# Kernel optimization log

Measured on AMD Instinct MI355X. Metric: run time of the kernel, lower is better.

Reference implementation:

```python
import jax, jax.numpy as jnp
import numpy as np

N_NODES = 50000
N_EDGES = 800000
IN_DIM = 16
HID = 128
OUT_DIM = 1
N_LAYERS = 2


def setup_inputs() -> dict:
    key = jax.random.key(0)
    ks = jax.random.split(key, 16)
    s = 0.05
    inp = {
        "edge_feats": jax.random.normal(ks[0], (N_EDGES, IN_DIM), jnp.float32),
        "node_feats": jax.random.normal(ks[1], (N_NODES, 4), jnp.float32),
        "src": jax.random.randint(ks[2], (N_EDGES,), 0, N_NODES, jnp.int32),
        "dst": jax.random.randint(ks[3], (N_EDGES,), 0, N_NODES, jnp.int32),
        # edge_embedding (dead in original forward, kept for faithfulness)
        "W_eemb": jax.random.normal(ks[4], (IN_DIM, HID), jnp.float32) * s,
        "b_eemb": jnp.zeros((HID,), jnp.float32),
        # node_embedding: Linear(4, hidden)
        "W_nemb": jax.random.normal(ks[5], (4, HID), jnp.float32) * s,
        "b_nemb": jnp.zeros((HID,), jnp.float32),
        # stacked GraphConv weights [n_layers, H, H]
        "gnn_W": jax.random.normal(ks[6], (N_LAYERS, HID, HID), jnp.float32) * s,
        "gnn_b": jnp.zeros((N_LAYERS, HID), jnp.float32),
        # output MLP
        "out_W1": jax.random.normal(ks[7], (HID, HID), jnp.float32) * s,
        "out_b1": jnp.zeros((HID,), jnp.float32),
        "out_W2": jax.random.normal(ks[8], (HID, OUT_DIM), jnp.float32) * s,
        "out_b2": jnp.zeros((OUT_DIM,), jnp.float32),
    }
    return inp


def reference(edge_feats, node_feats, src, dst, W_eemb, b_eemb, W_nemb, b_nemb,
              gnn_W, gnn_b, out_W1, out_b1, out_W2, out_b2):
    ones = jnp.ones((src.shape[0],), jnp.float32)
    deg_out = jnp.clip(jax.ops.segment_sum(ones, src, num_segments=N_NODES), 1.0)
    deg_in = jnp.clip(jax.ops.segment_sum(ones, dst, num_segments=N_NODES), 1.0)
    norm_out = deg_out ** -0.5  # [N]
    norm_in = deg_in ** -0.5    # [N]

    # edge_embedding output is dead code in the original forward (overwritten)
    _h_e = edge_feats @ W_eemb + b_eemb

    h = node_feats @ W_nemb + b_nemb  # [N, H]
    for l in range(N_LAYERS):
        # DGL GraphConv norm='both': D_out^{-1/2} gather -> scatter-sum -> D_in^{-1/2} -> W, b
        hs = h * norm_out[:, None]
        agg = jax.ops.segment_sum(hs[src], dst, num_segments=N_NODES)  # [N, H]
        h = agg * norm_in[:, None]
        h = h @ gnn_W[l] + gnn_b[l]
        h = jax.nn.relu(h)

    edge_h = h[src] + h[dst]  # apply_edges UDF, [E, H]
    x = jax.nn.relu(edge_h @ out_W1 + out_b1)
    return x @ out_W2 + out_b2  # [E, OUT_DIM]
```

## Files before the change

### kernel.cpp

```cpp
#include <hip/hip_runtime.h>

#define N_NODES 50000
#define N_EDGES 800000
#define HID 128
#define NB 256
#define NPB 196
#define TP 136

typedef __attribute__((ext_vector_type(8))) _Float16 f16x8;
typedef __attribute__((ext_vector_type(2))) _Float16 h2v;
typedef __attribute__((ext_vector_type(2))) __fp16 fp16v2;
typedef __attribute__((ext_vector_type(4))) float f32x4;
typedef __attribute__((ext_vector_type(2))) float f32x2;

__device__ __forceinline__ unsigned pkh(float a, float b) {
  union { fp16v2 h; unsigned u; } c;
  c.h = __builtin_amdgcn_cvt_pkrtz(a, b);
  return c.u;
}
__device__ __forceinline__ h2v u2h(unsigned u) {
  union { unsigned u; h2v h; } c;
  c.u = u;
  return c.h;
}
__device__ __forceinline__ f32x2 unpkh(unsigned u) {
  h2v h = u2h(u);
  f32x2 r;
  r[0] = (float)h[0];
  r[1] = (float)h[1];
  return r;
}
__device__ __forceinline__ short f2hs(float f) {
  union { _Float16 h; short s; } c;
  c.h = (_Float16)f;
  return c.s;
}
__device__ __forceinline__ unsigned hrelu_add(unsigned a, unsigned b) {
  h2v r = u2h(a) + u2h(b);
  h2v z = {(_Float16)0.f, (_Float16)0.f};
  r = __builtin_elementwise_max(r, z);
  union { h2v h; unsigned u; } c;
  c.h = r;
  return c.u;
}


__global__ __launch_bounds__(256) void p1_hist_kernel(
    const int* __restrict__ src, const int* __restrict__ dst,
    int* __restrict__ bcnt_d, int* __restrict__ bcnt_s) {
  __shared__ int hd[NB], hs[NB];
  int t = threadIdx.x;
  hd[t] = 0; hs[t] = 0;
  __syncthreads();
  for (int e = blockIdx.x * 256 + t; e < N_EDGES; e += gridDim.x * 256) {
    atomicAdd(&hd[dst[e] / NPB], 1);
    atomicAdd(&hs[src[e] / NPB], 1);
  }
  __syncthreads();
  if (hd[t]) atomicAdd(&bcnt_d[t], hd[t]);
  if (hs[t]) atomicAdd(&bcnt_s[t], hs[t]);
}

__global__ void p2_scan_prep_kernel(
    const int* __restrict__ bcnt_d, const int* __restrict__ bcnt_s,
    int* __restrict__ bofs_d, int* __restrict__ bofs_s,
    int* __restrict__ cur_d, int* __restrict__ cur_s,
    const float* __restrict__ Wa, const float* __restrict__ Wb,
    const float* __restrict__ Wc, const float* __restrict__ w2f,
    short* __restrict__ Wta, short* __restrict__ Wtb, short* __restrict__ Wtc,
    unsigned* __restrict__ w2h, short* __restrict__ h1bz) {
  int b = blockIdx.x;
  if (b > 0) {
    int t = (b - 1) * 256 + threadIdx.x;
    if (t < HID * HID) {
      int k = t >> 7, n = t & 127;
      Wta[n * HID + k] = f2hs(Wa[t]);
      Wtb[n * HID + k] = f2hs(Wb[t]);
      Wtc[n * HID + k] = f2hs(Wc[t]);
    }
    if (b == 1) {
      int t0 = threadIdx.x;
      if (t0 < 64) {
        w2h[t0] = pkh(w2f[2 * t0], w2f[2 * t0 + 1]);
      } else if (t0 < 128) {
        ((unsigned*)h1bz)[t0 - 64] = 0u;
      }
    }
    return;
  }
  __shared__ int s[NB];
  int t = threadIdx.x;
  int v = bcnt_d[t];
  s[t] = v;
  __syncthreads();
  for (int o = 1; o < NB; o <<= 1) {
    int x = (t >= o) ? s[t - o] : 0;
    __syncthreads();
    s[t] += x;
    __syncthreads();
  }
  int ofs = s[t] - v;
  bofs_d[t] = ofs; cur_d[t] = ofs;
  if (t == NB - 1) bofs_d[NB] = s[t];
  __syncthreads();
  v = bcnt_s[t];
  s[t] = v;
  __syncthreads();
  for (int o = 1; o < NB; o <<= 1) {
    int x = (t >= o) ? s[t - o] : 0;
    __syncthreads();
    s[t] += x;
    __syncthreads();
  }
  ofs = s[t] - v;
  bofs_s[t] = ofs; cur_s[t] = ofs;
  if (t == NB - 1) bofs_s[NB] = s[t];
}

__global__ __launch_bounds__(256) void p3_scatter_both_kernel(
    const int* __restrict__ src, const int* __restrict__ dst,
    int* __restrict__ cur_d, int* __restrict__ cur_s,
    int2* __restrict__ sdst, int* __restrict__ ssrc) {
  __shared__ int bcd[NB], bbd[NB], bcs[NB], bbs[NB];
  int t = threadIdx.x;
  int base = blockIdx.x * 2048;
  bcd[t] = 0; bcs[t] = 0;
  __syncthreads();
  int mybd[8], myrd[8], mys[8], myp[8], mybs[8], myrs[8];
#pragma unroll
  for (int u = 0; u < 8; ++u) {
    int e = base + u * 256 + t;
    mybd[u] = -1;
    if (e < N_EDGES) {
      int s = src[e], d = dst[e];
      int bd = d / NPB;
      mybd[u] = bd;
      myrd[u] = atomicAdd(&bcd[bd], 1);
      mys[u] = s;
      myp[u] = ((d - bd * NPB) << 20) | e;
      int bs = s / NPB;
      mybs[u] = bs;
      myrs[u] = atomicAdd(&bcs[bs], 1);
    }
  }
  __syncthreads();
  {
    int cd = bcd[t];
    if (cd) bbd[t] = atomicAdd(&cur_d[t], cd);
    int cs = bcs[t];
    if (cs) bbs[t] = atomicAdd(&cur_s[t], cs);
  }
  __syncthreads();
#pragma unroll
  for (int u = 0; u < 8; ++u) {
    if (mybd[u] >= 0) {
      sdst[bbd[mybd[u]] + myrd[u]] = make_int2(mys[u], myp[u]);
      ssrc[bbs[mybs[u]] + myrs[u]] = mys[u];
    }
  }
}

__global__ __launch_bounds__(256) void p45_kernel(
    const int2* __restrict__ sdst, const int* __restrict__ bofs_d,
    int* __restrict__ row_ofs, float* __restrict__ norm_in,
    int* __restrict__ csr_src, int* __restrict__ csr_eid, int* __restrict__ csr_dst,
    const int* __restrict__ ssrc, const int* __restrict__ bofs_s,
    float* __restrict__ norm_out) {
  __shared__ int hc[NB], sc[NB], cur[NB];
  int t = threadIdx.x;
  if (blockIdx.x >= NB) {
    int b = blockIdx.x - NB;
    int base = bofs_s[b], cnt = bofs_s[b + 1] - base;
    int lo = b * NPB;
    hc[t] = 0;
    __syncthreads();
    for (int i = t; i < cnt; i += 256) atomicAdd(&hc[ssrc[base + i] - lo], 1);
    __syncthreads();
    int node = lo + t;
    if (t < NPB && node < N_NODES) {
      int v = hc[t];
      norm_out[node] = rsqrtf((float)(v < 1 ? 1 : v));
    }
    return;
  }
  int b = blockIdx.x;
  int base = bofs_d[b], cnt = bofs_d[b + 1] - base;
  hc[t] = 0;
  __syncthreads();
  for (int i = t; i < cnt; i += 256) atomicAdd(&hc[sdst[base + i].y >> 20], 1);
  __syncthreads();
  int v = hc[t];
  sc[t] = v;
  __syncthreads();
  for (int o = 1; o < NB; o <<= 1) {
    int x = (t >= o) ? sc[t - o] : 0;
    __syncthreads();
    sc[t] += x;
    __syncthreads();
  }
  int ofs = sc[t] - v;
  int node = b * NPB + t;
  if (t < NPB && node < N_NODES) {
    row_ofs[node] = base + ofs;
    norm_in[node] = rsqrtf((float)(v < 1 ? 1 : v));
  }
  cur[t] = base + ofs;
  if (b == 0 && t == 0) row_ofs[N_NODES] = N_EDGES;
  __syncthreads();
  for (int i = t; i < cnt; i += 256) {
    int2 e = sdst[base + i];
    int loc = e.y >> 20;
    int pos = atomicAdd(&cur[loc], 1);
    csr_src[pos] = e.x;
    csr_eid[pos] = e.y & 0xFFFFF;
    csr_dst[pos] = b * NPB + loc;
  }
}


__global__ __launch_bounds__(256) void agg4_kernel(
    const float4* __restrict__ nf4, const float* __restrict__ no_,
    const int* __restrict__ csr_src, const int* __restrict__ row_ofs,
    float4* __restrict__ agg4, float* __restrict__ sno) {
  int wid = (blockIdx.x * blockDim.x + threadIdx.x) >> 6;
  int lane = threadIdx.x & 63;
  int g = lane >> 4, l = lane & 15;
  int v = wid * 4 + g;
  if (v >= N_NODES) return;
  int beg = row_ofs[v], end = row_ofs[v + 1];
  float ax = 0.f, ay = 0.f, az = 0.f, aw = 0.f, sn = 0.f;
  for (int i = beg + l; i < end; i += 16) {
    int s = csr_src[i];
    float w = no_[s];
    float4 n = nf4[s];
    ax += n.x * w; ay += n.y * w; az += n.z * w; aw += n.w * w;
    sn += w;
  }
#pragma unroll
  for (int o = 1; o < 16; o <<= 1) {
    ax += __shfl_xor(ax, o, 16);
    ay += __shfl_xor(ay, o, 16);
    az += __shfl_xor(az, o, 16);
    aw += __shfl_xor(aw, o, 16);
    sn += __shfl_xor(sn, o, 16);
  }
  if (l == 0) {
    agg4[v] = make_float4(ax, ay, az, aw);
    sno[v] = sn;
  }
}

__global__ __launch_bounds__(256) void gemm_l1_mfma(
    const float4* __restrict__ agg4, const float* __restrict__ sno,
    const float* __restrict__ ni_, const float* __restrict__ no_,
    const float* __restrict__ Wn, const float* __restrict__ bn,
    const short* __restrict__ Wt0, const float* __restrict__ b0,
    short* __restrict__ h1b, int nrows) {
  int t = threadIdx.x;
  int w = t >> 6, lane = t & 63;
  int m16 = lane & 15, quad = lane >> 4;
  int v0 = blockIdx.x * 64;
  int row = v0 + w * 16 + m16;
  bool rvalid = row < nrows;
  int rc = rvalid ? row : (nrows - 1);
  float4 a = agg4[rc];
  float sn = sno[rc], nin = ni_[rc];

  f16x8 xfr[4];
#pragma unroll
  for (int kc = 0; kc < 4; ++kc) {
    union { unsigned u[4]; f16x8 v; } cv;
#pragma unroll
    for (int jj = 0; jj < 4; ++jj) {
      int k0 = kc * 32 + quad * 8 + jj * 2;
      float x0 = (a.x * Wn[k0] + a.y * Wn[HID + k0] + a.z * Wn[2 * HID + k0] +
                  a.w * Wn[3 * HID + k0] + bn[k0] * sn) * nin;
      int k1 = k0 + 1;
      float x1 = (a.x * Wn[k1] + a.y * Wn[HID + k1] + a.z * Wn[2 * HID + k1] +
                  a.w * Wn[3 * HID + k1] + bn[k1] * sn) * nin;
      cv.u[jj] = pkh(x0, x1);
    }
    xfr[kc] = cv.v;
  }
  f32x4 acc[8];
#pragma unroll
  for (int nt = 0; nt < 8; ++nt) {
    acc[nt][0] = 0.f; acc[nt][1] = 0.f; acc[nt][2] = 0.f; acc[nt][3] = 0.f;
  }
#pragma unroll
  for (int nt = 0; nt < 8; ++nt) {
    const f16x8* Wr = (const f16x8*)(Wt0 + (size_t)(nt * 16 + m16) * HID);
#pragma unroll
    for (int kc = 0; kc < 4; ++kc)
      acc[nt] = __builtin_amdgcn_mfma_f32_16x16x32_f16(Wr[kc * 4 + quad], xfr[kc],
                                                       acc[nt], 0, 0, 0);
  }
  if (rvalid) {
    float nov = no_[row];
#pragma unroll
    for (int nt = 0; nt < 8; ++nt) {
      int nb = nt * 16 + quad * 4;
      float4 bv = *(const float4*)&b0[nb];
      float r0 = fmaxf(acc[nt][0] + bv.x, 0.f) * nov;
      float r1 = fmaxf(acc[nt][1] + bv.y, 0.f) * nov;
      float r2 = fmaxf(acc[nt][2] + bv.z, 0.f) * nov;
      float r3 = fmaxf(acc[nt][3] + bv.w, 0.f) * nov;
      uint2 pk;
      pk.x = pkh(r0, r1);
      pk.y = pkh(r2, r3);
      *(uint2*)(h1b + (size_t)row * HID + nb) = pk;
    }
  }
}

__global__ __launch_bounds__(256) void aggregate_kernel(
    const uint4* __restrict__ hb, const int* __restrict__ row_ofs,
    const int* __restrict__ csr_src, const float* __restrict__ ni_,
    uint4* __restrict__ Ab) {
  int v = (blockIdx.x * blockDim.x + threadIdx.x) >> 6;
  int lane = threadIdx.x & 63;
  if (v >= N_NODES) return;
  int beg = row_ofs[v], end = row_ofs[v + 1];
  int g = lane >> 4, l = lane & 15;
  f32x2 acc2[4];
#pragma unroll
  for (int j = 0; j < 4; ++j) acc2[j] = (f32x2){0.f, 0.f};
  for (int i = beg; i < end; i += 16) {
    int ss[4];
#pragma unroll
    for (int u = 0; u < 4; ++u) {
      int ii = i + 4 * u + g;
      ss[u] = (ii < end) ? csr_src[ii] : N_NODES;
    }
    uint4 X[4];
#pragma unroll
    for (int u = 0; u < 4; ++u) X[u] = hb[(size_t)ss[u] * 16 + l];
#pragma unroll
    for (int u = 0; u < 4; ++u) {
      acc2[0] += unpkh(X[u].x);
      acc2[1] += unpkh(X[u].y);
      acc2[2] += unpkh(X[u].z);
      acc2[3] += unpkh(X[u].w);
    }
  }
#pragma unroll
  for (int j = 0; j < 4; ++j) {
    acc2[j][0] += __shfl_xor(acc2[j][0], 16, 64);
    acc2[j][0] += __shfl_xor(acc2[j][0], 32, 64);
    acc2[j][1] += __shfl_xor(acc2[j][1], 16, 64);
    acc2[j][1] += __shfl_xor(acc2[j][1], 32, 64);
  }
  if (g == 0) {
    float n = ni_[v];
    uint4 pk;
    pk.x = pkh(acc2[0][0] * n, acc2[0][1] * n);
    pk.y = pkh(acc2[1][0] * n, acc2[1][1] * n);
    pk.z = pkh(acc2[2][0] * n, acc2[2][1] * n);
    pk.w = pkh(acc2[3][0] * n, acc2[3][1] * n);
    Ab[(size_t)v * 16 + l] = pk;
  }
}

__global__ __launch_bounds__(256) void gemm_dual_mfma(
    const short* __restrict__ Ab, const short* __restrict__ Wt0,
    const float* __restrict__ b0, const short* __restrict__ Wt1,
    const float* __restrict__ b1o, short* __restrict__ yb, int nrows) {
  __shared__ short T1s[4][16 * TP];
  int t = threadIdx.x;
  int w = t >> 6, lane = t & 63;
  int m16 = lane & 15, quad = lane >> 4;
  int v0 = blockIdx.x * 64;
  int row = v0 + w * 16 + m16;
  bool rvalid = row < nrows;
  int rc = rvalid ? row : (nrows - 1);

  f16x8 xfr[4];
  {
    const f16x8* Ar = (const f16x8*)(Ab + (size_t)rc * HID);
#pragma unroll
    for (int kc = 0; kc < 4; ++kc) xfr[kc] = Ar[kc * 4 + quad];
  }
  f32x4 acc[8];
#pragma unroll
  for (int nt = 0; nt < 8; ++nt) {
    acc[nt][0] = 0.f; acc[nt][1] = 0.f; acc[nt][2] = 0.f; acc[nt][3] = 0.f;
  }
#pragma unroll
  for (int nt = 0; nt < 8; ++nt) {
    const f16x8* Wr = (const f16x8*)(Wt0 + (size_t)(nt * 16 + m16) * HID);
#pragma unroll
    for (int kc = 0; kc < 4; ++kc)
      acc[nt] = __builtin_amdgcn_mfma_f32_16x16x32_f16(Wr[kc * 4 + quad], xfr[kc],
                                                       acc[nt], 0, 0, 0);
  }
  short* T1w = &T1s[w][0];
#pragma unroll
  for (int nt = 0; nt < 8; ++nt) {
    int nb = nt * 16 + quad * 4;
    float4 bv = *(const float4*)&b0[nb];
    float r0 = fmaxf(acc[nt][0] + bv.x, 0.f);
    float r1 = fmaxf(acc[nt][1] + bv.y, 0.f);
    float r2 = fmaxf(acc[nt][2] + bv.z, 0.f);
    float r3 = fmaxf(acc[nt][3] + bv.w, 0.f);
    uint2 pk;
    pk.x = pkh(r0, r1);
    pk.y = pkh(r2, r3);
    *(uint2*)&T1w[m16 * TP + nb] = pk;
    acc[nt][0] = 0.f; acc[nt][1] = 0.f; acc[nt][2] = 0.f; acc[nt][3] = 0.f;
  }
  __syncthreads();
  f16x8 tfr[4];
#pragma unroll
  for (int kc = 0; kc < 4; ++kc)
    tfr[kc] = *(const f16x8*)&T1w[m16 * TP + kc * 32 + quad * 8];
#pragma unroll
  for (int nt = 0; nt < 8; ++nt) {
    const f16x8* Wr = (const f16x8*)(Wt1 + (size_t)(nt * 16 + m16) * HID);
#pragma unroll
    for (int kc = 0; kc < 4; ++kc)
      acc[nt] = __builtin_amdgcn_mfma_f32_16x16x32_f16(Wr[kc * 4 + quad], tfr[kc],
                                                       acc[nt], 0, 0, 0);
  }
  if (rvalid) {
#pragma unroll
    for (int nt = 0; nt < 8; ++nt) {
      int nb = nt * 16 + quad * 4;
      float4 bv = *(const float4*)&b1o[nb];
      uint2 pk;
      pk.x = pkh(acc[nt][0] + 0.5f * bv.x, acc[nt][1] + 0.5f * bv.y);
      pk.y = pkh(acc[nt][2] + 0.5f * bv.z, acc[nt][3] + 0.5f * bv.w);
      *(uint2*)(yb + (size_t)row * HID + nb) = pk;
    }
  }
}

__global__ __launch_bounds__(256) void edge_out_mfma(
    const int* __restrict__ csr_src, const int* __restrict__ csr_dst,
    const int* __restrict__ csr_eid, const short* __restrict__ yb,
    const short* __restrict__ w2h16, const float* __restrict__ b2,
    float* __restrict__ out) {
  int t = threadIdx.x;
  int wv = (blockIdx.x * 256 + t) >> 6;
  int lane = t & 63;
  int m16 = lane & 15, quad = lane >> 4;
  int e0 = wv * 64;
  if (e0 >= N_EDGES) return;
  float ob2 = b2[0];

  f16x8 bfr[4];
#pragma unroll
  for (int kb = 0; kb < 4; ++kb)
    bfr[kb] = *(const f16x8*)(w2h16 + kb * 32 + quad * 8);

#pragma unroll
  for (int g = 0; g < 4; ++g) {
    int e = e0 + g * 16 + m16;
    int s = csr_src[e], d = csr_dst[e];
    const short* ys = yb + (size_t)s * HID + quad * 8;
    const short* yd = yb + (size_t)d * HID + quad * 8;
    f32x4 acc = {0.f, 0.f, 0.f, 0.f};
#pragma unroll
    for (int kb = 0; kb < 4; ++kb) {
      uint4 a = *(const uint4*)(ys + kb * 32);
      uint4 b = *(const uint4*)(yd + kb * 32);
      union { uint4 u; f16x8 v; } r;
      r.u.x = hrelu_add(a.x, b.x);
      r.u.y = hrelu_add(a.y, b.y);
      r.u.z = hrelu_add(a.z, b.z);
      r.u.w = hrelu_add(a.w, b.w);
      acc = __builtin_amdgcn_mfma_f32_16x16x32_f16(r.v, bfr[kb], acc, 0, 0, 0);
    }
    if (m16 == 0) {
      int eb = e0 + g * 16 + quad * 4;
#pragma unroll
      for (int r = 0; r < 4; ++r) {
        out[csr_eid[eb + r]] = acc[r] + ob2;
      }
    }
  }
}

extern "C" void kernel_launch(void* const* d_in, const int* in_sizes, int n_in,
                              void* d_out, int out_size, void* d_ws, size_t ws_size,
                              hipStream_t stream) {
  const float* node_feats = (const float*)d_in[1];
  const int*   src        = (const int*)d_in[2];
  const int*   dst        = (const int*)d_in[3];
  const float* W_nemb     = (const float*)d_in[6];
  const float* b_nemb     = (const float*)d_in[7];
  const float* gnn_W      = (const float*)d_in[8];
  const float* gnn_b      = (const float*)d_in[9];
  const float* out_W1     = (const float*)d_in[10];
  const float* out_b1     = (const float*)d_in[11];
  const float* out_W2     = (const float*)d_in[12];
  const float* out_b2     = (const float*)d_in[13];
  float* out = (float*)d_out;

  size_t off = 0;
  char* base = (char*)d_ws;
  auto alloc = [&](size_t nbytes) -> char* {
    off = (off + 255) & ~(size_t)255;
    char* p = base + off;
    off += nbytes;
    return p;
  };
  int*    bcnt2    = (int*)alloc(2 * NB * 4);
  int*    bofs_d   = (int*)alloc((NB + 1) * 4);
  int*    bofs_s   = (int*)alloc((NB + 1) * 4);
  int*    cur_d    = (int*)alloc(NB * 4);
  int*    cur_s    = (int*)alloc(NB * 4);
  float*  norm_out = (float*)alloc(N_NODES * 4);
  float*  norm_in  = (float*)alloc(N_NODES * 4);
  int*    row_ofs  = (int*)alloc((N_NODES + 1) * 4);
  int*    csr_src  = (int*)alloc((size_t)N_EDGES * 4);
  int*    csr_eid  = (int*)alloc((size_t)N_EDGES * 4);
  int*    csr_dst  = (int*)alloc((size_t)N_EDGES * 4);
  float4* agg4     = (float4*)alloc((size_t)N_NODES * 16);
  float*  sno      = (float*)alloc(N_NODES * 4);
  short*  Wta      = (short*)alloc((size_t)HID * HID * 2);
  short*  Wtb      = (short*)alloc((size_t)HID * HID * 2);
  short*  Wtc      = (short*)alloc((size_t)HID * HID * 2);
  unsigned* w2h    = (unsigned*)alloc(64 * 4);
  short*  h1b      = (short*)alloc((size_t)(N_NODES + 1) * HID * 2);
  short*  Ab       = (short*)alloc((size_t)N_NODES * HID * 2);
  short*  ybs      = (short*)alloc((size_t)N_NODES * HID * 2);
  int2*   sdst     = (int2*)Ab;
  int*    ssrc     = (int*)ybs;
  int*    bcnt_d   = bcnt2;
  int*    bcnt_s   = bcnt2 + NB;
  (void)ws_size; (void)n_in; (void)in_sizes; (void)out_size;

  (void)hipMemsetAsync(bcnt2, 0, 2 * NB * 4, stream);
  p1_hist_kernel<<<128, 256, 0, stream>>>(src, dst, bcnt_d, bcnt_s);
  p2_scan_prep_kernel<<<65, 256, 0, stream>>>(
      bcnt_d, bcnt_s, bofs_d, bofs_s, cur_d, cur_s,
      gnn_W, gnn_W + (size_t)HID * HID, out_W1, out_W2,
      Wta, Wtb, Wtc, w2h, h1b + (size_t)N_NODES * HID);
  p3_scatter_both_kernel<<<(N_EDGES + 2047) / 2048, 256, 0, stream>>>(
      src, dst, cur_d, cur_s, sdst, ssrc);
  p45_kernel<<<2 * NB, 256, 0, stream>>>(
      sdst, bofs_d, row_ofs, norm_in, csr_src, csr_eid, csr_dst,
      ssrc, bofs_s, norm_out);

  agg4_kernel<<<(N_NODES * 16 + 255) / 256, 256, 0, stream>>>(
      (const float4*)node_feats, norm_out, csr_src, row_ofs, agg4, sno);
  gemm_l1_mfma<<<(N_NODES + 63) / 64, 256, 0, stream>>>(
      agg4, sno, norm_in, norm_out, W_nemb, b_nemb, Wta, gnn_b, h1b, N_NODES);

  aggregate_kernel<<<(N_NODES * 64 + 255) / 256, 256, 0, stream>>>(
      (const uint4*)h1b, row_ofs, csr_src, norm_in, (uint4*)Ab);

  gemm_dual_mfma<<<(N_NODES + 63) / 64, 256, 0, stream>>>(
      Ab, Wtb, gnn_b + HID, Wtc, out_b1, ybs, N_NODES);

  edge_out_mfma<<<(N_EDGES / 64 + 3) / 4, 256, 0, stream>>>(
      csr_src, csr_dst, csr_eid, ybs, (const short*)w2h, out_b2, out);
}
```

Before: 302.7 us.

## Bucket edges into 8 source-node chunks for cache-local edge output gathers

During CSR construction, edges are also scattered into 8 buckets by source node range using a global per-bucket cursor seeded from the source block offsets. The final edge kernel then processes edges chunk by chunk, with block index interleaved across chunks, so the source-row gathers of the ybs buffer touch a narrower node range and can hit cache better. It also hoists all eight row loads ahead of the MFMA loop to raise memory-level parallelism. This costs extra atomics and writes of three arrays in p45, and assumes ECB*256 covers the largest chunk.

```diff
diff --git a/kernel.cpp b/kernel.cpp
--- a/kernel.cpp
+++ b/kernel.cpp
@@ -6,6 +6,7 @@
 #define NB 256
 #define NPB 196
 #define TP 136
+#define ECB 408
 
 typedef __attribute__((ext_vector_type(8))) _Float16 f16x8;
 typedef __attribute__((ext_vector_type(2))) _Float16 h2v;
@@ -65,6 +66,7 @@
     const int* __restrict__ bcnt_d, const int* __restrict__ bcnt_s,
     int* __restrict__ bofs_d, int* __restrict__ bofs_s,
     int* __restrict__ cur_d, int* __restrict__ cur_s,
+    int* __restrict__ gcur8,
     const float* __restrict__ Wa, const float* __restrict__ Wb,
     const float* __restrict__ Wc, const float* __restrict__ w2f,
     short* __restrict__ Wta, short* __restrict__ Wtb, short* __restrict__ Wtc,
@@ -114,6 +116,7 @@
   }
   ofs = s[t] - v;
   bofs_s[t] = ofs; cur_s[t] = ofs;
+  if ((t & 31) == 0) gcur8[t >> 5] = ofs;
   if (t == NB - 1) bofs_s[NB] = s[t];
 }
 
@@ -163,10 +166,13 @@
 __global__ __launch_bounds__(256) void p45_kernel(
     const int2* __restrict__ sdst, const int* __restrict__ bofs_d,
     int* __restrict__ row_ofs, float* __restrict__ norm_in,
-    int* __restrict__ csr_src, int* __restrict__ csr_eid, int* __restrict__ csr_dst,
+    int* __restrict__ csr_src, int* __restrict__ csr_eid,
+    int* __restrict__ gcur8, int* __restrict__ es8, int* __restrict__ ed8,
+    int* __restrict__ eid8,
     const int* __restrict__ ssrc, const int* __restrict__ bofs_s,
     float* __restrict__ norm_out) {
   __shared__ int hc[NB], sc[NB], cur[NB];
+  __shared__ int h8[8], b8[8];
   int t = threadIdx.x;
   if (blockIdx.x >= NB) {
     int b = blockIdx.x - NB;
@@ -186,11 +192,20 @@
   int b = blockIdx.x;
   int base = bofs_d[b], cnt = bofs_d[b + 1] - base;
   hc[t] = 0;
-  __syncthreads();
-  for (int i = t; i < cnt; i += 256) atomicAdd(&hc[sdst[base + i].y >> 20], 1);
+  if (t < 8) h8[t] = 0;
+  __syncthreads();
+  for (int i = t; i < cnt; i += 256) {
+    int2 e = sdst[base + i];
+    atomicAdd(&hc[e.y >> 20], 1);
+    atomicAdd(&h8[(e.x / NPB) >> 5], 1);
+  }
   __syncthreads();
   int v = hc[t];
   sc[t] = v;
+  if (t < 8) {
+    b8[t] = atomicAdd(&gcur8[t], h8[t]);
+    h8[t] = 0;
+  }
   __syncthreads();
   for (int o = 1; o < NB; o <<= 1) {
     int x = (t >= o) ? sc[t - o] : 0;
@@ -213,7 +228,11 @@
     int pos = atomicAdd(&cur[loc], 1);
     csr_src[pos] = e.x;
     csr_eid[pos] = e.y & 0xFFFFF;
-    csr_dst[pos] = b * NPB + loc;
+    int k = (e.x / NPB) >> 5;
+    int sp = b8[k] + atomicAdd(&h8[k], 1);
+    es8[sp] = e.x;
+    ed8[sp] = b * NPB + loc;
+    eid8[sp] = e.y & 0xFFFFF;
   }
 }
 
@@ -435,16 +454,19 @@
 }
 
 __global__ __launch_bounds__(256) void edge_out_mfma(
-    const int* __restrict__ csr_src, const int* __restrict__ csr_dst,
-    const int* __restrict__ csr_eid, const short* __restrict__ yb,
-    const short* __restrict__ w2h16, const float* __restrict__ b2,
-    float* __restrict__ out) {
-  int t = threadIdx.x;
-  int wv = (blockIdx.x * 256 + t) >> 6;
+    const int* __restrict__ es8, const int* __restrict__ ed8,
+    const int* __restrict__ eid8, const int* __restrict__ bofs_s,
+    const short* __restrict__ yb, const short* __restrict__ w2h16,
+    const float* __restrict__ b2, float* __restrict__ out) {
+  int t = threadIdx.x;
+  int chunk = blockIdx.x & 7;
+  int slot = blockIdx.x >> 3;
+  int cbeg = bofs_s[chunk * 32];
+  int cend = bofs_s[chunk * 32 + 32];
+  int e0 = cbeg + slot * 256 + (t >> 6) * 64;
+  if (e0 >= cend) return;
   int lane = t & 63;
   int m16 = lane & 15, quad = lane >> 4;
-  int e0 = wv * 64;
-  if (e0 >= N_EDGES) return;
   float ob2 = b2[0];
 
   f16x8 bfr[4];
@@ -455,26 +477,32 @@
 #pragma unroll
   for (int g = 0; g < 4; ++g) {
     int e = e0 + g * 16 + m16;
-    int s = csr_src[e], d = csr_dst[e];
+    int ec = (e < cend) ? e : cbeg;
+    int s = es8[ec], d = ed8[ec];
     const short* ys = yb + (size_t)s * HID + quad * 8;
     const short* yd = yb + (size_t)d * HID + quad * 8;
+    uint4 A[4], B[4];
+#pragma unroll
+    for (int kb = 0; kb < 4; ++kb) {
+      A[kb] = *(const uint4*)(ys + kb * 32);
+      B[kb] = *(const uint4*)(yd + kb * 32);
+    }
     f32x4 acc = {0.f, 0.f, 0.f, 0.f};
 #pragma unroll
     for (int kb = 0; kb < 4; ++kb) {
-      uint4 a = *(const uint4*)(ys + kb * 32);
-      uint4 b = *(const uint4*)(yd + kb * 32);
       union { uint4 u; f16x8 v; } r;
-      r.u.x = hrelu_add(a.x, b.x);
-      r.u.y = hrelu_add(a.y, b.y);
-      r.u.z = hrelu_add(a.z, b.z);
-      r.u.w = hrelu_add(a.w, b.w);
+      r.u.x = hrelu_add(A[kb].x, B[kb].x);
+      r.u.y = hrelu_add(A[kb].y, B[kb].y);
+      r.u.z = hrelu_add(A[kb].z, B[kb].z);
+      r.u.w = hrelu_add(A[kb].w, B[kb].w);
       acc = __builtin_amdgcn_mfma_f32_16x16x32_f16(r.v, bfr[kb], acc, 0, 0, 0);
     }
     if (m16 == 0) {
       int eb = e0 + g * 16 + quad * 4;
 #pragma unroll
       for (int r = 0; r < 4; ++r) {
-        out[csr_eid[eb + r]] = acc[r] + ob2;
+        int ee = eb + r;
+        if (ee < cend) out[eid8[ee]] = acc[r] + ob2;
       }
     }
   }
@@ -509,12 +537,15 @@
   int*    bofs_s   = (int*)alloc((NB + 1) * 4);
   int*    cur_d    = (int*)alloc(NB * 4);
   int*    cur_s    = (int*)alloc(NB * 4);
+  int*    gcur8    = (int*)alloc(8 * 4);
   float*  norm_out = (float*)alloc(N_NODES * 4);
   float*  norm_in  = (float*)alloc(N_NODES * 4);
   int*    row_ofs  = (int*)alloc((N_NODES + 1) * 4);
   int*    csr_src  = (int*)alloc((size_t)N_EDGES * 4);
   int*    csr_eid  = (int*)alloc((size_t)N_EDGES * 4);
-  int*    csr_dst  = (int*)alloc((size_t)N_EDGES * 4);
+  int*    es8      = (int*)alloc((size_t)N_EDGES * 4);
+  int*    ed8      = (int*)alloc((size_t)N_EDGES * 4);
+  int*    eid8     = (int*)alloc((size_t)N_EDGES * 4);
   float4* agg4     = (float4*)alloc((size_t)N_NODES * 16);
   float*  sno      = (float*)alloc(N_NODES * 4);
   short*  Wta      = (short*)alloc((size_t)HID * HID * 2);
@@ -533,14 +564,14 @@
   (void)hipMemsetAsync(bcnt2, 0, 2 * NB * 4, stream);
   p1_hist_kernel<<<128, 256, 0, stream>>>(src, dst, bcnt_d, bcnt_s);
   p2_scan_prep_kernel<<<65, 256, 0, stream>>>(
-      bcnt_d, bcnt_s, bofs_d, bofs_s, cur_d, cur_s,
+      bcnt_d, bcnt_s, bofs_d, bofs_s, cur_d, cur_s, gcur8,
       gnn_W, gnn_W + (size_t)HID * HID, out_W1, out_W2,
       Wta, Wtb, Wtc, w2h, h1b + (size_t)N_NODES * HID);
   p3_scatter_both_kernel<<<(N_EDGES + 2047) / 2048, 256, 0, stream>>>(
       src, dst, cur_d, cur_s, sdst, ssrc);
   p45_kernel<<<2 * NB, 256, 0, stream>>>(
-      sdst, bofs_d, row_ofs, norm_in, csr_src, csr_eid, csr_dst,
-      ssrc, bofs_s, norm_out);
+      sdst, bofs_d, row_ofs, norm_in, csr_src, csr_eid,
+      gcur8, es8, ed8, eid8, ssrc, bofs_s, norm_out);
 
   agg4_kernel<<<(N_NODES * 16 + 255) / 256, 256, 0, stream>>>(
       (const float4*)node_feats, norm_out, csr_src, row_ofs, agg4, sno);
@@ -553,6 +584,6 @@
   gemm_dual_mfma<<<(N_NODES + 63) / 64, 256, 0, stream>>>(
       Ab, Wtb, gnn_b + HID, Wtc, out_b1, ybs, N_NODES);
 
-  edge_out_mfma<<<(N_EDGES / 64 + 3) / 4, 256, 0, stream>>>(
-      csr_src, csr_dst, csr_eid, ybs, (const short*)w2h, out_b2, out);
-}
+  edge_out_mfma<<<8 * ECB, 256, 0, stream>>>(
+      es8, ed8, eid8, bofs_s, ybs, (const short*)w2h, out_b2, out);
+}
```

New measurement: 319.9 us. 1.06x slower.

## Fuse layer-2 neighbor aggregation into dual GEMM kernel via shared memory

Applied to the files above, without the earlier changes.

Merges the gather-aggregate kernel into the dual-MFMA GEMM kernel: each wave aggregates 16 nodes sequentially into an LDS tile, then feeds the tile directly to the MFMA GEMMs. This removes the global write and read of the aggregated fp16 node matrix and one kernel launch. In exchange, each wave now processes its 16 nodes serially, so far fewer waves are in flight to hide gather latency. The sdst scratch buffer gets its own allocation since it can no longer alias the removed buffer.

```diff
diff --git a/kernel.cpp b/kernel.cpp
--- a/kernel.cpp
+++ b/kernel.cpp
@@ -6,6 +6,7 @@
 #define NB 256
 #define NPB 196
 #define TP 136
+#define AP 132
 
 typedef __attribute__((ext_vector_type(8))) _Float16 f16x8;
 typedef __attribute__((ext_vector_type(2))) _Float16 h2v;
@@ -313,73 +314,71 @@
   }
 }
 
-__global__ __launch_bounds__(256) void aggregate_kernel(
+__global__ __launch_bounds__(256) void agg_gemm_dual(
     const uint4* __restrict__ hb, const int* __restrict__ row_ofs,
     const int* __restrict__ csr_src, const float* __restrict__ ni_,
-    uint4* __restrict__ Ab) {
-  int v = (blockIdx.x * blockDim.x + threadIdx.x) >> 6;
-  int lane = threadIdx.x & 63;
-  if (v >= N_NODES) return;
-  int beg = row_ofs[v], end = row_ofs[v + 1];
+    const short* __restrict__ Wt0, const float* __restrict__ b0,
+    const short* __restrict__ Wt1, const float* __restrict__ b1o,
+    short* __restrict__ yb, int nrows) {
+  __shared__ short Asl[4][16 * AP];
+  __shared__ short T1s[4][16 * TP];
+  int t = threadIdx.x;
+  int w = t >> 6, lane = t & 63;
   int g = lane >> 4, l = lane & 15;
-  f32x2 acc2[4];
-#pragma unroll
-  for (int j = 0; j < 4; ++j) acc2[j] = (f32x2){0.f, 0.f};
-  for (int i = beg; i < end; i += 16) {
-    int ss[4];
-#pragma unroll
-    for (int u = 0; u < 4; ++u) {
-      int ii = i + 4 * u + g;
-      ss[u] = (ii < end) ? csr_src[ii] : N_NODES;
-    }
-    uint4 X[4];
-#pragma unroll
-    for (int u = 0; u < 4; ++u) X[u] = hb[(size_t)ss[u] * 16 + l];
-#pragma unroll
-    for (int u = 0; u < 4; ++u) {
-      acc2[0] += unpkh(X[u].x);
-      acc2[1] += unpkh(X[u].y);
-      acc2[2] += unpkh(X[u].z);
-      acc2[3] += unpkh(X[u].w);
-    }
-  }
-#pragma unroll
-  for (int j = 0; j < 4; ++j) {
-    acc2[j][0] += __shfl_xor(acc2[j][0], 16, 64);
-    acc2[j][0] += __shfl_xor(acc2[j][0], 32, 64);
-    acc2[j][1] += __shfl_xor(acc2[j][1], 16, 64);
-    acc2[j][1] += __shfl_xor(acc2[j][1], 32, 64);
-  }
-  if (g == 0) {
-    float n = ni_[v];
-    uint4 pk;
-    pk.x = pkh(acc2[0][0] * n, acc2[0][1] * n);
-    pk.y = pkh(acc2[1][0] * n, acc2[1][1] * n);
-    pk.z = pkh(acc2[2][0] * n, acc2[2][1] * n);
-    pk.w = pkh(acc2[3][0] * n, acc2[3][1] * n);
-    Ab[(size_t)v * 16 + l] = pk;
-  }
-}
-
-__global__ __launch_bounds__(256) void gemm_dual_mfma(
-    const short* __restrict__ Ab, const short* __restrict__ Wt0,
-    const float* __restrict__ b0, const short* __restrict__ Wt1,
-    const float* __restrict__ b1o, short* __restrict__ yb, int nrows) {
-  __shared__ short T1s[4][16 * TP];
-  int t = threadIdx.x;
-  int w = t >> 6, lane = t & 63;
-  int m16 = lane & 15, quad = lane >> 4;
-  int v0 = blockIdx.x * 64;
-  int row = v0 + w * 16 + m16;
-  bool rvalid = row < nrows;
-  int rc = rvalid ? row : (nrows - 1);
-
+  int v0 = blockIdx.x * 64 + w * 16;
+  short* Aw = &Asl[w][0];
+
+  for (int j = 0; j < 16; ++j) {
+    int v = v0 + j;
+    f32x2 acc2[4];
+#pragma unroll
+    for (int q = 0; q < 4; ++q) acc2[q] = (f32x2){0.f, 0.f};
+    if (v < nrows) {
+      int beg = row_ofs[v], end = row_ofs[v + 1];
+      for (int i = beg; i < end; i += 16) {
+        int ss[4];
+#pragma unroll
+        for (int u = 0; u < 4; ++u) {
+          int ii = i + 4 * u + g;
+          ss[u] = (ii < end) ? csr_src[ii] : N_NODES;
+        }
+        uint4 X[4];
+#pragma unroll
+        for (int u = 0; u < 4; ++u) X[u] = hb[(size_t)ss[u] * 16 + l];
+#pragma unroll
+        for (int u = 0; u < 4; ++u) {
+          acc2[0] += unpkh(X[u].x);
+          acc2[1] += unpkh(X[u].y);
+          acc2[2] += unpkh(X[u].z);
+          acc2[3] += unpkh(X[u].w);
+        }
+      }
+#pragma unroll
+      for (int q = 0; q < 4; ++q) {
+        acc2[q][0] += __shfl_xor(acc2[q][0], 16, 64);
+        acc2[q][0] += __shfl_xor(acc2[q][0], 32, 64);
+        acc2[q][1] += __shfl_xor(acc2[q][1], 16, 64);
+        acc2[q][1] += __shfl_xor(acc2[q][1], 32, 64);
+      }
+    }
+    if (g == 0) {
+      float n = (v < nrows) ? ni_[v] : 0.f;
+      uint4 pk;
+      pk.x = pkh(acc2[0][0] * n, acc2[0][1] * n);
+      pk.y = pkh(acc2[1][0] * n, acc2[1][1] * n);
+      pk.z = pkh(acc2[2][0] * n, acc2[2][1] * n);
+      pk.w = pkh(acc2[3][0] * n, acc2[3][1] * n);
+      *(uint4*)&Aw[j * AP + l * 8] = pk;
+    }
+  }
+  __syncthreads();
+
+  int m16 = l, quad = g;
+  int row = v0 + m16;
   f16x8 xfr[4];
-  {
-    const f16x8* Ar = (const f16x8*)(Ab + (size_t)rc * HID);
-#pragma unroll
-    for (int kc = 0; kc < 4; ++kc) xfr[kc] = Ar[kc * 4 + quad];
-  }
+#pragma unroll
+  for (int kc = 0; kc < 4; ++kc)
+    xfr[kc] = *(const f16x8*)&Aw[m16 * AP + kc * 32 + quad * 8];
   f32x4 acc[8];
 #pragma unroll
   for (int nt = 0; nt < 8; ++nt) {
@@ -421,7 +420,7 @@
       acc[nt] = __builtin_amdgcn_mfma_f32_16x16x32_f16(Wr[kc * 4 + quad], tfr[kc],
                                                        acc[nt], 0, 0, 0);
   }
-  if (rvalid) {
+  if (row < nrows) {
 #pragma unroll
     for (int nt = 0; nt < 8; ++nt) {
       int nb = nt * 16 + quad * 4;
@@ -515,6 +514,7 @@
   int*    csr_src  = (int*)alloc((size_t)N_EDGES * 4);
   int*    csr_eid  = (int*)alloc((size_t)N_EDGES * 4);
   int*    csr_dst  = (int*)alloc((size_t)N_EDGES * 4);
+  int2*   sdst     = (int2*)alloc((size_t)N_EDGES * 8);
   float4* agg4     = (float4*)alloc((size_t)N_NODES * 16);
   float*  sno      = (float*)alloc(N_NODES * 4);
   short*  Wta      = (short*)alloc((size_t)HID * HID * 2);
@@ -522,9 +522,7 @@
   short*  Wtc      = (short*)alloc((size_t)HID * HID * 2);
   unsigned* w2h    = (unsigned*)alloc(64 * 4);
   short*  h1b      = (short*)alloc((size_t)(N_NODES + 1) * HID * 2);
-  short*  Ab       = (short*)alloc((size_t)N_NODES * HID * 2);
   short*  ybs      = (short*)alloc((size_t)N_NODES * HID * 2);
-  int2*   sdst     = (int2*)Ab;
   int*    ssrc     = (int*)ybs;
   int*    bcnt_d   = bcnt2;
   int*    bcnt_s   = bcnt2 + NB;
@@ -547,11 +545,9 @@
   gemm_l1_mfma<<<(N_NODES + 63) / 64, 256, 0, stream>>>(
       agg4, sno, norm_in, norm_out, W_nemb, b_nemb, Wta, gnn_b, h1b, N_NODES);
 
-  aggregate_kernel<<<(N_NODES * 64 + 255) / 256, 256, 0, stream>>>(
-      (const uint4*)h1b, row_ofs, csr_src, norm_in, (uint4*)Ab);
-
-  gemm_dual_mfma<<<(N_NODES + 63) / 64, 256, 0, stream>>>(
-      Ab, Wtb, gnn_b + HID, Wtc, out_b1, ybs, N_NODES);
+  agg_gemm_dual<<<(N_NODES + 63) / 64, 256, 0, stream>>>(
+      (const uint4*)h1b, row_ofs, csr_src, norm_in,
+      Wtb, gnn_b + HID, Wtc, out_b1, ybs, N_NODES);
 
   edge_out_mfma<<<(N_EDGES / 64 + 3) / 4, 256, 0, stream>>>(
       csr_src, csr_dst, csr_eid, ybs, (const short*)w2h, out_b2, out);
```

New measurement: 316.5 us. 4.5% more time.
